# Kernel tuning notes

Measured on AMD Instinct MI355X. Metric: run time of the kernel, lower is better.

The kernel has to match this reference:

```python
import jax, jax.numpy as jnp
import numpy as np

N, E, D, H, C, G, L = 50000, 1250000, 128, 64, 10, 128, 2


def setup_inputs() -> dict:
    key = jax.random.key(0)
    ks = jax.random.split(key, 18)
    s = lambda fan_in: 1.0 / np.sqrt(fan_in)
    inp = {
        "x": jax.random.normal(ks[0], (N, D), dtype=jnp.float32),
        "edge_index": jax.random.randint(ks[1], (2, E), 0, N, dtype=jnp.int64),
        "batch": jnp.sort(jax.random.randint(ks[2], (N,), 0, G, dtype=jnp.int64)),
        # node embedding MLP (D->H->H)
        "emb_w1": jax.random.uniform(ks[3], (D, H), jnp.float32, -s(D), s(D)),
        "emb_b1": jnp.zeros((H,), jnp.float32),
        "emb_w2": jax.random.uniform(ks[4], (H, H), jnp.float32, -s(H), s(H)),
        "emb_b2": jnp.zeros((H,), jnp.float32),
        # per-conv-block params, stacked over L layers
        "rel_w": jax.random.uniform(ks[5], (L, H, H), jnp.float32, -s(H), s(H)),
        "rel_b": jnp.zeros((L, H), jnp.float32),
        "root_w": jax.random.uniform(ks[6], (L, H, H), jnp.float32, -s(H), s(H)),
        "post_w1": jax.random.uniform(ks[7], (L, H, H), jnp.float32, -s(H), s(H)),
        "post_b1": jnp.zeros((L, H), jnp.float32),
        "post_w2": jax.random.uniform(ks[8], (L, H, H), jnp.float32, -s(H), s(H)),
        "post_b2": jnp.zeros((L, H), jnp.float32),
        # classifier
        "cls_w": jax.random.uniform(ks[9], (H, C), jnp.float32, -s(H), s(H)),
        "cls_b": jnp.zeros((C,), jnp.float32),
    }
    return inp


def _mlp(h, w1, b1, w2, b2):
    # Linear -> relu -> (dropout: identity in eval) -> Linear
    return jax.nn.relu(h @ w1 + b1) @ w2 + b2


def reference(x, edge_index, batch, emb_w1, emb_b1, emb_w2, emb_b2,
              rel_w, rel_b, root_w, post_w1, post_b1, post_w2, post_b2,
              cls_w, cls_b):
    src, dst = edge_index[0], edge_index[1]
    h = _mlp(x, emb_w1, emb_b1, emb_w2, emb_b2)  # [N,H]
    deg = jax.ops.segment_sum(jnp.ones((E,), h.dtype), dst, num_segments=N)
    inv_deg = 1.0 / jnp.maximum(deg, 1.0)  # mean aggregation, isolated nodes -> 0
    for l in range(L):
        agg = jax.ops.segment_sum(h[src], dst, num_segments=N) * inv_deg[:, None]
        h = agg @ rel_w[l] + rel_b[l] + h @ root_w[l]  # GraphConv (lin_root bias-free)
        h = _mlp(h, post_w1[l], post_b1[l], post_w2[l], post_b2[l])
        h = jax.nn.relu(h)  # dropout is identity in eval
    cnt = jax.ops.segment_sum(jnp.ones((N,), h.dtype), batch, num_segments=G)
    pooled = jax.ops.segment_sum(h, batch, num_segments=G) / jnp.maximum(cnt, 1.0)[:, None]
    return pooled @ cls_w + cls_b  # [G,C]
```

## Files before the change

kernel.cpp:

```cpp
#include <hip/hip_runtime.h>

typedef unsigned int u32;
typedef unsigned short u16;

#define NN 50000
#define EE 1250000
#define DD 128
#define HH 64
#define NCLS 10
#define NG 128
#define MAXDEG 80

#define NTILES ((NN + 63) / 64)

#define PBUK 392
#define SBLK 128
#define CHUNK ((EE + SBLK - 1) / SBLK)
#define NDP  (PBUK * 128)

#define WT_LO  (8 * 4096)
#define WT_E1  (16 * 4096)
#define WT_E1L (WT_E1 + 8192)
#define WT_E2  (WT_E1 + 16384)
#define WT_E2L (WT_E2 + 4096)
#define WT_TOT (WT_E2 + 8192)


__device__ __forceinline__ u32 f2bf(float f) {
    u32 u = __float_as_uint(f);
    return (u + 0x7FFFu + ((u >> 16) & 1u)) >> 16;
}
__device__ __forceinline__ float bf2f(u16 v) {
    return __uint_as_float(((u32)v) << 16);
}

typedef __attribute__((ext_vector_type(8))) short bf16x8;
typedef __attribute__((ext_vector_type(4))) float f32x4;


__global__ __launch_bounds__(256) void k_wprep(
    const float* __restrict__ rel_w, const float* __restrict__ root_w,
    const float* __restrict__ pw1, const float* __restrict__ pw2,
    const float* __restrict__ ew1, const float* __restrict__ ew2,
    u16* __restrict__ wtb) {
    __shared__ float ldsf[128 * 65];
    const int t = threadIdx.x;
    const int m = blockIdx.x;
    if (m < 8) {
        const int layer = m >> 2, which = m & 3;
        const float* srcw =
            (which == 0 ? rel_w : which == 1 ? root_w : which == 2 ? pw1 : pw2)
            + (size_t)layer * HH * HH;
        #pragma unroll
        for (int r = 0; r < 16; ++r) {
            int idx = r * 256 + t;
            int k = idx >> 6, n = idx & 63;
            ldsf[k * 65 + n] = srcw[idx];
        }
        __syncthreads();
        #pragma unroll
        for (int r = 0; r < 16; ++r) {
            int idx = r * 256 + t;
            int n = idx >> 6, k = idx & 63;
            float v = ldsf[k * 65 + n];
            u16 hi = (u16)f2bf(v);
            u16 lo = (u16)f2bf(v - bf2f(hi));
            wtb[m * 4096 + idx] = hi;
            wtb[WT_LO + m * 4096 + idx] = lo;
        }
    } else if (m == 8) {
        #pragma unroll
        for (int r = 0; r < 32; ++r) {
            int idx = r * 256 + t;
            int k = idx >> 6, n = idx & 63;
            ldsf[k * 65 + n] = ew1[idx];
        }
        __syncthreads();
        #pragma unroll
        for (int r = 0; r < 32; ++r) {
            int idx = r * 256 + t;
            int n = idx >> 7, k = idx & 127;
            float v = ldsf[k * 65 + n];
            u16 hi = (u16)f2bf(v);
            u16 lo = (u16)f2bf(v - bf2f(hi));
            wtb[WT_E1 + idx] = hi;
            wtb[WT_E1L + idx] = lo;
        }
    } else {
        #pragma unroll
        for (int r = 0; r < 16; ++r) {
            int idx = r * 256 + t;
            int k = idx >> 6, n = idx & 63;
            ldsf[k * 65 + n] = ew2[idx];
        }
        __syncthreads();
        #pragma unroll
        for (int r = 0; r < 16; ++r) {
            int idx = r * 256 + t;
            int n = idx >> 6, k = idx & 63;
            float v = ldsf[k * 65 + n];
            u16 hi = (u16)f2bf(v);
            u16 lo = (u16)f2bf(v - bf2f(hi));
            wtb[WT_E2 + idx] = hi;
            wtb[WT_E2L + idx] = lo;
        }
    }
}


__global__ __launch_bounds__(256) void k_embed_psort(
    const float* __restrict__ x,
    const float* __restrict__ b1, const float* __restrict__ b2,
    const u16* __restrict__ wtb,
    u16* __restrict__ hb,
    const int* __restrict__ ei, u32* __restrict__ bedges,
    int* __restrict__ gboff, int* __restrict__ ghist) {
    __shared__ __align__(16) char smem[2 * 64 * 72 * 2];
    const int t = threadIdx.x;

    if (blockIdx.x < NTILES) {
        u16* acts0 = (u16*)smem;
        u16* acts1 = (u16*)smem + 64 * 72;
        const int l = t & 63;
        const int lr = l & 15, lg = l >> 4;
        const int rowb = (t >> 6) * 16;
        const int nb = blockIdx.x * 64;
        int nodeA = nb + rowb + lr;
        if (nodeA >= NN) nodeA = NN - 1;
        const float* xp = x + (size_t)nodeA * DD + lg * 8;

        f32x4 acc[4];
        #pragma unroll
        for (int tt = 0; tt < 4; ++tt) {
            float b = b1[tt * 16 + lr];
            acc[tt] = (f32x4){b, b, b, b};
        }
        #pragma unroll
        for (int kc = 0; kc < 4; ++kc) {
            float4 v0 = *(const float4*)(xp + kc * 32);
            float4 v1 = *(const float4*)(xp + kc * 32 + 4);
            float vv[8] = {v0.x, v0.y, v0.z, v0.w, v1.x, v1.y, v1.z, v1.w};
            bf16x8 xh, xl;
            #pragma unroll
            for (int j = 0; j < 8; ++j) {
                u16 hi = (u16)f2bf(vv[j]);
                xh[j] = (short)hi;
                xl[j] = (short)(u16)f2bf(vv[j] - bf2f(hi));
            }
            #pragma unroll
            for (int tt = 0; tt < 4; ++tt) {
                const u16* ph = wtb + WT_E1 + (tt * 16 + lr) * 128 + kc * 32 + lg * 8;
                const u16* pl = wtb + WT_E1L + (tt * 16 + lr) * 128 + kc * 32 + lg * 8;
                bf16x8 wh = *(const bf16x8*)ph;
                bf16x8 wl = *(const bf16x8*)pl;
                acc[tt] = __builtin_amdgcn_mfma_f32_16x16x32_bf16(xh, wh, acc[tt], 0, 0, 0);
                acc[tt] = __builtin_amdgcn_mfma_f32_16x16x32_bf16(xl, wh, acc[tt], 0, 0, 0);
                acc[tt] = __builtin_amdgcn_mfma_f32_16x16x32_bf16(xh, wl, acc[tt], 0, 0, 0);
            }
        }
        #pragma unroll
        for (int tt = 0; tt < 4; ++tt)
            #pragma unroll
            for (int r = 0; r < 4; ++r) {
                float v = fmaxf(acc[tt][r], 0.0f);
                u16 hi = (u16)f2bf(v);
                u16 lo = (u16)f2bf(v - bf2f(hi));
                acts0[(rowb + lg * 4 + r) * 72 + tt * 16 + lr] = hi;
                acts1[(rowb + lg * 4 + r) * 72 + tt * 16 + lr] = lo;
            }
        __syncthreads();

        bf16x8 c0h = *(const bf16x8*)&acts0[(rowb + lr) * 72 + lg * 8];
        bf16x8 c1h = *(const bf16x8*)&acts0[(rowb + lr) * 72 + 32 + lg * 8];
        bf16x8 c0l = *(const bf16x8*)&acts1[(rowb + lr) * 72 + lg * 8];
        bf16x8 c1l = *(const bf16x8*)&acts1[(rowb + lr) * 72 + 32 + lg * 8];
        f32x4 acc2[4];
        #pragma unroll
        for (int tt = 0; tt < 4; ++tt) {
            float b = b2[tt * 16 + lr];
            acc2[tt] = (f32x4){b, b, b, b};
        }
        #pragma unroll
        for (int tt = 0; tt < 4; ++tt) {
            const u16* ph = wtb + WT_E2 + (tt * 16 + lr) * 64 + lg * 8;
            const u16* pl = wtb + WT_E2L + (tt * 16 + lr) * 64 + lg * 8;
            bf16x8 wh0 = *(const bf16x8*)ph;
            bf16x8 wh1 = *(const bf16x8*)(ph + 32);
            bf16x8 wl0 = *(const bf16x8*)pl;
            bf16x8 wl1 = *(const bf16x8*)(pl + 32);
            acc2[tt] = __builtin_amdgcn_mfma_f32_16x16x32_bf16(c0h, wh0, acc2[tt], 0, 0, 0);
            acc2[tt] = __builtin_amdgcn_mfma_f32_16x16x32_bf16(c1h, wh1, acc2[tt], 0, 0, 0);
            acc2[tt] = __builtin_amdgcn_mfma_f32_16x16x32_bf16(c0l, wh0, acc2[tt], 0, 0, 0);
            acc2[tt] = __builtin_amdgcn_mfma_f32_16x16x32_bf16(c1l, wh1, acc2[tt], 0, 0, 0);
            acc2[tt] = __builtin_amdgcn_mfma_f32_16x16x32_bf16(c0h, wl0, acc2[tt], 0, 0, 0);
            acc2[tt] = __builtin_amdgcn_mfma_f32_16x16x32_bf16(c1h, wl1, acc2[tt], 0, 0, 0);
        }
        #pragma unroll
        for (int tt = 0; tt < 4; ++tt)
            #pragma unroll
            for (int r = 0; r < 4; ++r) {
                int node = nb + rowb + lg * 4 + r;
                if (node < NN)
                    hb[(size_t)node * HH + tt * 16 + lr] = (u16)f2bf(acc2[tt][r]);
            }
    } else {
        int* hist  = (int*)smem;
        int* boffS = hist + PBUK;
        int* wsum  = boffS + PBUK;
        const int cb = blockIdx.x - NTILES;
        const int base = cb * CHUNK;
        const int n = min(CHUNK, EE - base);

        for (int b = t; b < PBUK; b += 256) hist[b] = 0;
        __syncthreads();
        for (int i = t; i < n; i += 256) {
            int src = ei[base + i];
            int dst = ei[EE + base + i];
            if ((unsigned)src < NN && (unsigned)dst < NN)
                atomicAdd(&hist[dst >> 7], 1);
        }
        __syncthreads();
        int v = 0, h0 = 0;
        if (t < PBUK / 2) { h0 = hist[2 * t]; v = h0 + hist[2 * t + 1]; }
        int lane = t & 63, wd = t >> 6;
        int incl = v;
        #pragma unroll
        for (int d = 1; d < 64; d <<= 1) {
            int tt = __shfl_up(incl, d);
            if (lane >= d) incl += tt;
        }
        if (lane == 63) wsum[wd] = incl;
        __syncthreads();
        int woff = 0;
        for (int w = 0; w < wd; ++w) woff += wsum[w];
        if (t < PBUK / 2) {
            int excl = woff + incl - v;
            boffS[2 * t] = excl;
            boffS[2 * t + 1] = excl + h0;
        }
        __syncthreads();
        for (int b = t; b < PBUK; b += 256) {
            gboff[cb * PBUK + b] = boffS[b];
            ghist[cb * PBUK + b] = hist[b];
        }
        __syncthreads();
        for (int b = t; b < PBUK; b += 256) hist[b] = 0;
        __syncthreads();
        for (int i = t; i < n; i += 256) {
            int src = ei[base + i];
            int dst = ei[EE + base + i];
            if ((unsigned)src < NN && (unsigned)dst < NN) {
                int b = dst >> 7;
                int p = atomicAdd(&hist[b], 1);
                bedges[base + boffS[b] + p] = ((u32)src << 7) | (u32)(dst & 127);
            }
        }
    }
}


__global__ __launch_bounds__(256) void k_adj(const u32* __restrict__ bedges,
                                             const int* __restrict__ gboff,
                                             const int* __restrict__ ghist,
                                             u16* __restrict__ slots,
                                             int* __restrict__ deg,
                                             float* __restrict__ pooled,
                                             u16* __restrict__ hb) {
    __shared__ u16 ls[128 * MAXDEG];
    __shared__ int lc[128];
    const int b = blockIdx.x, t = threadIdx.x;
    const int lane = t & 63, wid = t >> 6;
    if (b < (NG * HH) / 256) pooled[b * 256 + t] = 0.0f;
    if (b == 0 && t < 32) ((u32*)hb)[NN * (HH / 2) + t] = 0;
    if (t < 128) lc[t] = 0;
    {
        const u32 sent = ((u32)NN << 16) | (u32)NN;
        u32* lsu = (u32*)ls;
        for (int i = t; i < 128 * MAXDEG / 2; i += 256) lsu[i] = sent;
    }
    __syncthreads();
    for (int sb = wid; sb < SBLK; sb += 4) {
        int off = gboff[sb * PBUK + b];
        int cnt = ghist[sb * PBUK + b];
        int gbase = sb * CHUNK + off;
        for (int i = lane; i < cnt; i += 64) {
            u32 p = bedges[gbase + i];
            int o = (int)(p & 127u);
            int src = (int)(p >> 7);
            int pos = atomicAdd(&lc[o], 1);
            if (pos < MAXDEG) ls[o * MAXDEG + pos] = (u16)src;
        }
    }
    __syncthreads();
    u32* gs = (u32*)(slots + (size_t)b * 128 * MAXDEG);
    const u32* lsu = (const u32*)ls;
    for (int i = t; i < 128 * MAXDEG / 2; i += 256) gs[i] = lsu[i];
    if (t < 128) deg[b * 128 + t] = lc[t];
}


__global__ __launch_bounds__(256) void k_agg(
    const u16* __restrict__ hb, const int* __restrict__ deg,
    const u16* __restrict__ slots, u16* __restrict__ aggb) {
    const int wid = threadIdx.x >> 6, lane = threadIdx.x & 63;
    const int half = lane >> 5, fl = lane & 31;
    const int n0 = blockIdx.x * 8 + wid * 2;
    if (n0 >= NN) return;
    const int n = n0 + half;
    const bool valid = n < NN;
    const int d = valid ? deg[n] : 0;
    const int m = min(d, MAXDEG);
    const int mp = (m + 15) & ~15;
    const u32* row = (const u32*)(slots + (size_t)n * MAXDEG);
    float s0 = 0.0f, s1 = 0.0f;
    for (int e = 0; e < mp; e += 16) {
        const u32* rp = row + (e >> 1);
        uint4 i0 = *(const uint4*)rp;
        uint4 i1 = *(const uint4*)(rp + 4);
        u32 v0 = *(const u32*)(hb + (size_t)(i0.x & 0xffffu) * HH + 2 * fl);
        u32 v1 = *(const u32*)(hb + (size_t)(i0.x >> 16)    * HH + 2 * fl);
        u32 v2 = *(const u32*)(hb + (size_t)(i0.y & 0xffffu) * HH + 2 * fl);
        u32 v3 = *(const u32*)(hb + (size_t)(i0.y >> 16)    * HH + 2 * fl);
        u32 v4 = *(const u32*)(hb + (size_t)(i0.z & 0xffffu) * HH + 2 * fl);
        u32 v5 = *(const u32*)(hb + (size_t)(i0.z >> 16)    * HH + 2 * fl);
        u32 v6 = *(const u32*)(hb + (size_t)(i0.w & 0xffffu) * HH + 2 * fl);
        u32 v7 = *(const u32*)(hb + (size_t)(i0.w >> 16)    * HH + 2 * fl);
        u32 v8 = *(const u32*)(hb + (size_t)(i1.x & 0xffffu) * HH + 2 * fl);
        u32 v9 = *(const u32*)(hb + (size_t)(i1.x >> 16)    * HH + 2 * fl);
        u32 va = *(const u32*)(hb + (size_t)(i1.y & 0xffffu) * HH + 2 * fl);
        u32 vb = *(const u32*)(hb + (size_t)(i1.y >> 16)    * HH + 2 * fl);
        u32 vc = *(const u32*)(hb + (size_t)(i1.z & 0xffffu) * HH + 2 * fl);
        u32 vd = *(const u32*)(hb + (size_t)(i1.z >> 16)    * HH + 2 * fl);
        u32 ve = *(const u32*)(hb + (size_t)(i1.w & 0xffffu) * HH + 2 * fl);
        u32 vf = *(const u32*)(hb + (size_t)(i1.w >> 16)    * HH + 2 * fl);
        s0 += ((bf2f((u16)(v0 & 0xffffu)) + bf2f((u16)(v1 & 0xffffu)))
             + (bf2f((u16)(v2 & 0xffffu)) + bf2f((u16)(v3 & 0xffffu))))
            + ((bf2f((u16)(v4 & 0xffffu)) + bf2f((u16)(v5 & 0xffffu)))
             + (bf2f((u16)(v6 & 0xffffu)) + bf2f((u16)(v7 & 0xffffu))));
        s0 += ((bf2f((u16)(v8 & 0xffffu)) + bf2f((u16)(v9 & 0xffffu)))
             + (bf2f((u16)(va & 0xffffu)) + bf2f((u16)(vb & 0xffffu))))
            + ((bf2f((u16)(vc & 0xffffu)) + bf2f((u16)(vd & 0xffffu)))
             + (bf2f((u16)(ve & 0xffffu)) + bf2f((u16)(vf & 0xffffu))));
        s1 += ((bf2f((u16)(v0 >> 16)) + bf2f((u16)(v1 >> 16)))
             + (bf2f((u16)(v2 >> 16)) + bf2f((u16)(v3 >> 16))))
            + ((bf2f((u16)(v4 >> 16)) + bf2f((u16)(v5 >> 16)))
             + (bf2f((u16)(v6 >> 16)) + bf2f((u16)(v7 >> 16))));
        s1 += ((bf2f((u16)(v8 >> 16)) + bf2f((u16)(v9 >> 16)))
             + (bf2f((u16)(va >> 16)) + bf2f((u16)(vb >> 16))))
            + ((bf2f((u16)(vc >> 16)) + bf2f((u16)(vd >> 16)))
             + (bf2f((u16)(ve >> 16)) + bf2f((u16)(vf >> 16))));
    }
    if (valid) {
        float inv = 1.0f / (float)max(d, 1);
        u32 p = f2bf(s0 * inv) | (f2bf(s1 * inv) << 16);
        ((u32*)aggb)[(size_t)n * (HH / 2) + fl] = p;
    }
}


__global__ __launch_bounds__(256) void k_dense(
    u16* __restrict__ hb, const u16* __restrict__ aggb,
    const u16* __restrict__ wt,
    const float* __restrict__ relb,
    const float* __restrict__ pb1, const float* __restrict__ pb2,
    const int* __restrict__ batch, float* __restrict__ pooled, int do_pool) {
    __shared__ __align__(16) u16 acts[2][64][72];
    const int t = threadIdx.x;
    const int w = t >> 6;
    const int l = t & 63;
    const int lr = l & 15, lg = l >> 4;
    const int rowb = w * 16;
    const int nb = blockIdx.x * 64;
    int nodeA = nb + rowb + lr;
    if (nodeA >= NN) nodeA = NN - 1;

    const u16* w_rel = wt;
    const u16* w_root = wt + 4096;
    const u16* w_p1  = wt + 2 * 4096;
    const u16* w_p2  = wt + 3 * 4096;

    const u16* agp = aggb + (size_t)nodeA * HH + lg * 8;
    const u16* hbp = hb   + (size_t)nodeA * HH + lg * 8;
    bf16x8 a0 = *(const bf16x8*)agp;
    bf16x8 a1 = *(const bf16x8*)(agp + 32);
    bf16x8 h0 = *(const bf16x8*)hbp;
    bf16x8 h1 = *(const bf16x8*)(hbp + 32);

    f32x4 acc[4];
    #pragma unroll
    for (int tt = 0; tt < 4; ++tt) {
        float b = relb[tt * 16 + lr];
        acc[tt] = (f32x4){b, b, b, b};
    }
    #pragma unroll
    for (int tt = 0; tt < 4; ++tt) {
        const u16* pr = w_rel  + (tt * 16 + lr) * 64 + lg * 8;
        const u16* po = w_root + (tt * 16 + lr) * 64 + lg * 8;
        acc[tt] = __builtin_amdgcn_mfma_f32_16x16x32_bf16(a0, *(const bf16x8*)pr,                acc[tt], 0, 0, 0);
        acc[tt] = __builtin_amdgcn_mfma_f32_16x16x32_bf16(a1, *(const bf16x8*)(pr + 32),         acc[tt], 0, 0, 0);
        acc[tt] = __builtin_amdgcn_mfma_f32_16x16x32_bf16(a0, *(const bf16x8*)(pr + WT_LO),      acc[tt], 0, 0, 0);
        acc[tt] = __builtin_amdgcn_mfma_f32_16x16x32_bf16(a1, *(const bf16x8*)(pr + WT_LO + 32), acc[tt], 0, 0, 0);
        acc[tt] = __builtin_amdgcn_mfma_f32_16x16x32_bf16(h0, *(const bf16x8*)po,                acc[tt], 0, 0, 0);
        acc[tt] = __builtin_amdgcn_mfma_f32_16x16x32_bf16(h1, *(const bf16x8*)(po + 32),         acc[tt], 0, 0, 0);
        acc[tt] = __builtin_amdgcn_mfma_f32_16x16x32_bf16(h0, *(const bf16x8*)(po + WT_LO),      acc[tt], 0, 0, 0);
        acc[tt] = __builtin_amdgcn_mfma_f32_16x16x32_bf16(h1, *(const bf16x8*)(po + WT_LO + 32), acc[tt], 0, 0, 0);
    }
    #pragma unroll
    for (int tt = 0; tt < 4; ++tt)
        #pragma unroll
        for (int r = 0; r < 4; ++r)
            acts[0][rowb + lg * 4 + r][tt * 16 + lr] = (u16)f2bf(acc[tt][r]);
    __syncthreads();

    bf16x8 c0 = *(const bf16x8*)&acts[0][rowb + lr][lg * 8];
    bf16x8 c1 = *(const bf16x8*)&acts[0][rowb + lr][32 + lg * 8];
    f32x4 acc2[4];
    #pragma unroll
    for (int tt = 0; tt < 4; ++tt) {
        float b = pb1[tt * 16 + lr];
        acc2[tt] = (f32x4){b, b, b, b};
    }
    #pragma unroll
    for (int tt = 0; tt < 4; ++tt) {
        const u16* pr = w_p1 + (tt * 16 + lr) * 64 + lg * 8;
        acc2[tt] = __builtin_amdgcn_mfma_f32_16x16x32_bf16(c0, *(const bf16x8*)pr,                acc2[tt], 0, 0, 0);
        acc2[tt] = __builtin_amdgcn_mfma_f32_16x16x32_bf16(c1, *(const bf16x8*)(pr + 32),         acc2[tt], 0, 0, 0);
        acc2[tt] = __builtin_amdgcn_mfma_f32_16x16x32_bf16(c0, *(const bf16x8*)(pr + WT_LO),      acc2[tt], 0, 0, 0);
        acc2[tt] = __builtin_amdgcn_mfma_f32_16x16x32_bf16(c1, *(const bf16x8*)(pr + WT_LO + 32), acc2[tt], 0, 0, 0);
    }
    #pragma unroll
    for (int tt = 0; tt < 4; ++tt)
        #pragma unroll
        for (int r = 0; r < 4; ++r)
            acts[1][rowb + lg * 4 + r][tt * 16 + lr] = (u16)f2bf(fmaxf(acc2[tt][r], 0.0f));
    __syncthreads();

    bf16x8 d0 = *(const bf16x8*)&acts[1][rowb + lr][lg * 8];
    bf16x8 d1 = *(const bf16x8*)&acts[1][rowb + lr][32 + lg * 8];
    f32x4 acc3[4];
    #pragma unroll
    for (int tt = 0; tt < 4; ++tt) {
        float b = pb2[tt * 16 + lr];
        acc3[tt] = (f32x4){b, b, b, b};
    }
    #pragma unroll
    for (int tt = 0; tt < 4; ++tt) {
        const u16* pr = w_p2 + (tt * 16 + lr) * 64 + lg * 8;
        acc3[tt] = __builtin_amdgcn_mfma_f32_16x16x32_bf16(d0, *(const bf16x8*)pr,                acc3[tt], 0, 0, 0);
        acc3[tt] = __builtin_amdgcn_mfma_f32_16x16x32_bf16(d1, *(const bf16x8*)(pr + 32),         acc3[tt], 0, 0, 0);
        acc3[tt] = __builtin_amdgcn_mfma_f32_16x16x32_bf16(d0, *(const bf16x8*)(pr + WT_LO),      acc3[tt], 0, 0, 0);
        acc3[tt] = __builtin_amdgcn_mfma_f32_16x16x32_bf16(d1, *(const bf16x8*)(pr + WT_LO + 32), acc3[tt], 0, 0, 0);
    }

    if (!do_pool) {
        #pragma unroll
        for (int tt = 0; tt < 4; ++tt)
            #pragma unroll
            for (int r = 0; r < 4; ++r) {
                int node = nb + rowb + lg * 4 + r;
                if (node < NN)
                    hb[(size_t)node * HH + tt * 16 + lr] = (u16)f2bf(fmaxf(acc3[tt][r], 0.0f));
            }
    } else {
        #pragma unroll
        for (int tt = 0; tt < 4; ++tt)
            #pragma unroll
            for (int r = 0; r < 4; ++r)
                acts[0][rowb + lg * 4 + r][tt * 16 + lr] = (u16)f2bf(fmaxf(acc3[tt][r], 0.0f));
        __syncthreads();
        if (t < HH) {
            const int f = t;
            const int n1 = min(64, NN - nb);
            int cur = batch[nb];
            float s = 0.0f;
            for (int i = 0; i < n1; ++i) {
                int g = batch[nb + i];
                if (g != cur) {
                    if ((unsigned)cur < NG) atomicAdd(&pooled[cur * HH + f], s);
                    s = 0.0f; cur = g;
                }
                s += bf2f(acts[0][i][f]);
            }
            if ((unsigned)cur < NG) atomicAdd(&pooled[cur * HH + f], s);
        }
    }
}


__global__ void k_cls(const float* __restrict__ pooled, const int* __restrict__ batch,
                      const float* __restrict__ w, const float* __restrict__ b,
                      float* __restrict__ out) {
    const int g = blockIdx.x;
    const int t = threadIdx.x;
    if (t >= NCLS) return;
    int lo = 0, hi = NN;
    while (lo < hi) { int mid = (lo + hi) >> 1; if (batch[mid] < g) lo = mid + 1; else hi = mid; }
    const int beg = lo;
    lo = 0; hi = NN;
    while (lo < hi) { int mid = (lo + hi) >> 1; if (batch[mid] < g + 1) lo = mid + 1; else hi = mid; }
    const int cnt = lo - beg;
    const float inv = 1.0f / (float)max(cnt, 1);
    float o = b[t];
    #pragma unroll 8
    for (int k = 0; k < HH; ++k) o += pooled[g * HH + k] * inv * w[k * NCLS + t];
    out[g * NCLS + t] = o;
}


extern "C" void kernel_launch(void* const* d_in, const int* in_sizes, int n_in,
                              void* d_out, int out_size, void* d_ws, size_t ws_size,
                              hipStream_t stream) {
    const float* x      = (const float*)d_in[0];
    const int*   ei     = (const int*)d_in[1];
    const int*   batch  = (const int*)d_in[2];
    const float* emb_w1 = (const float*)d_in[3];
    const float* emb_b1 = (const float*)d_in[4];
    const float* emb_w2 = (const float*)d_in[5];
    const float* emb_b2 = (const float*)d_in[6];
    const float* rel_w  = (const float*)d_in[7];
    const float* rel_b  = (const float*)d_in[8];
    const float* root_w = (const float*)d_in[9];
    const float* pw1    = (const float*)d_in[10];
    const float* pb1    = (const float*)d_in[11];
    const float* pw2    = (const float*)d_in[12];
    const float* pb2    = (const float*)d_in[13];
    const float* cls_w  = (const float*)d_in[14];
    const float* cls_b  = (const float*)d_in[15];
    float* out = (float*)d_out;

    char* ws = (char*)d_ws;
    size_t off = 0;
    auto alloc = [&](size_t bytes) -> void* {
        off = (off + 255) & ~(size_t)255;
        void* p = ws + off;
        off += bytes;
        return p;
    };
    u16*   hb     = (u16*)alloc((size_t)(NN + 1) * HH * 2);
    u16*   aggb   = (u16*)alloc((size_t)NN * HH * 2);
    u32*   bedges = (u32*)aggb;
    u16*   slots  = (u16*)alloc((size_t)NDP * MAXDEG * 2);
    int*   deg    = (int*)alloc((size_t)NDP * 4);
    int*   gboff  = (int*)alloc((size_t)SBLK * PBUK * 4);
    int*   ghist  = (int*)alloc((size_t)SBLK * PBUK * 4);
    float* pooled = (float*)alloc((size_t)NG * HH * 4);
    u16*   wtb    = (u16*)alloc((size_t)WT_TOT * 2);

    k_wprep<<<10, 256, 0, stream>>>(rel_w, root_w, pw1, pw2, emb_w1, emb_w2, wtb);
    k_embed_psort<<<NTILES + SBLK, 256, 0, stream>>>(
        x, emb_b1, emb_b2, wtb, hb, ei, bedges, gboff, ghist);
    k_adj<<<PBUK, 256, 0, stream>>>(bedges, gboff, ghist, slots, deg, pooled, hb);
    k_agg<<<(NN + 7) / 8, 256, 0, stream>>>(hb, deg, slots, aggb);
    k_dense<<<NTILES, 256, 0, stream>>>(hb, aggb, wtb, rel_b, pb1, pb2, batch, pooled, 0);
    k_agg<<<(NN + 7) / 8, 256, 0, stream>>>(hb, deg, slots, aggb);
    k_dense<<<NTILES, 256, 0, stream>>>(hb, aggb, wtb + 4 * 4096,
                                        rel_b + HH, pb1 + HH, pb2 + HH,
                                        batch, pooled, 1);
    k_cls<<<NG, 64, 0, stream>>>(pooled, batch, cls_w, cls_b, out);
}
```

Baseline: 285.9 us.

## Restructure neighbor aggregation to one wave per node with 16-byte gathers

The aggregation kernel now assigns one 64-lane wave per node. Each lane loads 8 bf16 features (16 bytes) of one of 8 neighbors at a time, and the partial sums are reduced across lanes with xor shuffles. This replaces the previous scheme, where half-waves did 4-byte gathers over 16 neighbors per iteration. The intent is wider, more efficient memory transactions and less padding waste for low-degree nodes, at the cost of a shuffle reduction and more blocks. Separately, the edge bucketing loops in the partition-sort kernel are unrolled by four so each thread has more edge-index loads in flight.

```diff
diff --git a/kernel.cpp b/kernel.cpp
--- a/kernel.cpp
+++ b/kernel.cpp
@@ -213,11 +213,17 @@
 
         for (int b = t; b < PBUK; b += 256) hist[b] = 0;
         __syncthreads();
-        for (int i = t; i < n; i += 256) {
-            int src = ei[base + i];
-            int dst = ei[EE + base + i];
-            if ((unsigned)src < NN && (unsigned)dst < NN)
-                atomicAdd(&hist[dst >> 7], 1);
+        for (int i0 = t; i0 < n; i0 += 1024) {
+            const int i1 = i0 + 256, i2 = i0 + 512, i3 = i0 + 768;
+            int sA = ei[base + i0], dA = ei[EE + base + i0];
+            int sB = -1, dB = 0, sC = -1, dC = 0, sD = -1, dD = 0;
+            if (i1 < n) { sB = ei[base + i1]; dB = ei[EE + base + i1]; }
+            if (i2 < n) { sC = ei[base + i2]; dC = ei[EE + base + i2]; }
+            if (i3 < n) { sD = ei[base + i3]; dD = ei[EE + base + i3]; }
+            if ((unsigned)sA < NN && (unsigned)dA < NN) atomicAdd(&hist[dA >> 7], 1);
+            if ((unsigned)sB < NN && (unsigned)dB < NN) atomicAdd(&hist[dB >> 7], 1);
+            if ((unsigned)sC < NN && (unsigned)dC < NN) atomicAdd(&hist[dC >> 7], 1);
+            if ((unsigned)sD < NN && (unsigned)dD < NN) atomicAdd(&hist[dD >> 7], 1);
         }
         __syncthreads();
         int v = 0, h0 = 0;
@@ -246,13 +252,32 @@
         __syncthreads();
         for (int b = t; b < PBUK; b += 256) hist[b] = 0;
         __syncthreads();
-        for (int i = t; i < n; i += 256) {
-            int src = ei[base + i];
-            int dst = ei[EE + base + i];
-            if ((unsigned)src < NN && (unsigned)dst < NN) {
-                int b = dst >> 7;
+        for (int i0 = t; i0 < n; i0 += 1024) {
+            const int i1 = i0 + 256, i2 = i0 + 512, i3 = i0 + 768;
+            int sA = ei[base + i0], dA = ei[EE + base + i0];
+            int sB = -1, dB = 0, sC = -1, dC = 0, sD = -1, dD = 0;
+            if (i1 < n) { sB = ei[base + i1]; dB = ei[EE + base + i1]; }
+            if (i2 < n) { sC = ei[base + i2]; dC = ei[EE + base + i2]; }
+            if (i3 < n) { sD = ei[base + i3]; dD = ei[EE + base + i3]; }
+            if ((unsigned)sA < NN && (unsigned)dA < NN) {
+                int b = dA >> 7;
                 int p = atomicAdd(&hist[b], 1);
-                bedges[base + boffS[b] + p] = ((u32)src << 7) | (u32)(dst & 127);
+                bedges[base + boffS[b] + p] = ((u32)sA << 7) | (u32)(dA & 127);
+            }
+            if ((unsigned)sB < NN && (unsigned)dB < NN) {
+                int b = dB >> 7;
+                int p = atomicAdd(&hist[b], 1);
+                bedges[base + boffS[b] + p] = ((u32)sB << 7) | (u32)(dB & 127);
+            }
+            if ((unsigned)sC < NN && (unsigned)dC < NN) {
+                int b = dC >> 7;
+                int p = atomicAdd(&hist[b], 1);
+                bedges[base + boffS[b] + p] = ((u32)sC << 7) | (u32)(dC & 127);
+            }
+            if ((unsigned)sD < NN && (unsigned)dD < NN) {
+                int b = dD >> 7;
+                int p = atomicAdd(&hist[b], 1);
+                bedges[base + boffS[b] + p] = ((u32)sD << 7) | (u32)(dD & 127);
             }
         }
     }
@@ -303,57 +328,35 @@
     const u16* __restrict__ hb, const int* __restrict__ deg,
     const u16* __restrict__ slots, u16* __restrict__ aggb) {
     const int wid = threadIdx.x >> 6, lane = threadIdx.x & 63;
-    const int half = lane >> 5, fl = lane & 31;
-    const int n0 = blockIdx.x * 8 + wid * 2;
-    if (n0 >= NN) return;
-    const int n = n0 + half;
-    const bool valid = n < NN;
-    const int d = valid ? deg[n] : 0;
+    const int n = blockIdx.x * 4 + wid;
+    if (n >= NN) return;
+    const int d = deg[n];
     const int m = min(d, MAXDEG);
-    const int mp = (m + 15) & ~15;
-    const u32* row = (const u32*)(slots + (size_t)n * MAXDEG);
-    float s0 = 0.0f, s1 = 0.0f;
-    for (int e = 0; e < mp; e += 16) {
-        const u32* rp = row + (e >> 1);
-        uint4 i0 = *(const uint4*)rp;
-        uint4 i1 = *(const uint4*)(rp + 4);
-        u32 v0 = *(const u32*)(hb + (size_t)(i0.x & 0xffffu) * HH + 2 * fl);
-        u32 v1 = *(const u32*)(hb + (size_t)(i0.x >> 16)    * HH + 2 * fl);
-        u32 v2 = *(const u32*)(hb + (size_t)(i0.y & 0xffffu) * HH + 2 * fl);
-        u32 v3 = *(const u32*)(hb + (size_t)(i0.y >> 16)    * HH + 2 * fl);
-        u32 v4 = *(const u32*)(hb + (size_t)(i0.z & 0xffffu) * HH + 2 * fl);
-        u32 v5 = *(const u32*)(hb + (size_t)(i0.z >> 16)    * HH + 2 * fl);
-        u32 v6 = *(const u32*)(hb + (size_t)(i0.w & 0xffffu) * HH + 2 * fl);
-        u32 v7 = *(const u32*)(hb + (size_t)(i0.w >> 16)    * HH + 2 * fl);
-        u32 v8 = *(const u32*)(hb + (size_t)(i1.x & 0xffffu) * HH + 2 * fl);
-        u32 v9 = *(const u32*)(hb + (size_t)(i1.x >> 16)    * HH + 2 * fl);
-        u32 va = *(const u32*)(hb + (size_t)(i1.y & 0xffffu) * HH + 2 * fl);
-        u32 vb = *(const u32*)(hb + (size_t)(i1.y >> 16)    * HH + 2 * fl);
-        u32 vc = *(const u32*)(hb + (size_t)(i1.z & 0xffffu) * HH + 2 * fl);
-        u32 vd = *(const u32*)(hb + (size_t)(i1.z >> 16)    * HH + 2 * fl);
-        u32 ve = *(const u32*)(hb + (size_t)(i1.w & 0xffffu) * HH + 2 * fl);
-        u32 vf = *(const u32*)(hb + (size_t)(i1.w >> 16)    * HH + 2 * fl);
-        s0 += ((bf2f((u16)(v0 & 0xffffu)) + bf2f((u16)(v1 & 0xffffu)))
-             + (bf2f((u16)(v2 & 0xffffu)) + bf2f((u16)(v3 & 0xffffu))))
-            + ((bf2f((u16)(v4 & 0xffffu)) + bf2f((u16)(v5 & 0xffffu)))
-             + (bf2f((u16)(v6 & 0xffffu)) + bf2f((u16)(v7 & 0xffffu))));
-        s0 += ((bf2f((u16)(v8 & 0xffffu)) + bf2f((u16)(v9 & 0xffffu)))
-             + (bf2f((u16)(va & 0xffffu)) + bf2f((u16)(vb & 0xffffu))))
-            + ((bf2f((u16)(vc & 0xffffu)) + bf2f((u16)(vd & 0xffffu)))
-             + (bf2f((u16)(ve & 0xffffu)) + bf2f((u16)(vf & 0xffffu))));
-        s1 += ((bf2f((u16)(v0 >> 16)) + bf2f((u16)(v1 >> 16)))
-             + (bf2f((u16)(v2 >> 16)) + bf2f((u16)(v3 >> 16))))
-            + ((bf2f((u16)(v4 >> 16)) + bf2f((u16)(v5 >> 16)))
-             + (bf2f((u16)(v6 >> 16)) + bf2f((u16)(v7 >> 16))));
-        s1 += ((bf2f((u16)(v8 >> 16)) + bf2f((u16)(v9 >> 16)))
-             + (bf2f((u16)(va >> 16)) + bf2f((u16)(vb >> 16))))
-            + ((bf2f((u16)(vc >> 16)) + bf2f((u16)(vd >> 16)))
-             + (bf2f((u16)(ve >> 16)) + bf2f((u16)(vf >> 16))));
-    }
-    if (valid) {
+    const int mp = (m + 7) & ~7;
+    const int eg = lane >> 3;
+    const int fo = (lane & 7) * 8;
+    const u16* row = slots + (size_t)n * MAXDEG;
+    float s[8] = {0, 0, 0, 0, 0, 0, 0, 0};
+    for (int e = 0; e < mp; e += 8) {
+        int src = row[e + eg];
+        uint4 v = *(const uint4*)(hb + (size_t)src * HH + fo);
+        s[0] += bf2f((u16)(v.x & 0xffffu)); s[1] += bf2f((u16)(v.x >> 16));
+        s[2] += bf2f((u16)(v.y & 0xffffu)); s[3] += bf2f((u16)(v.y >> 16));
+        s[4] += bf2f((u16)(v.z & 0xffffu)); s[5] += bf2f((u16)(v.z >> 16));
+        s[6] += bf2f((u16)(v.w & 0xffffu)); s[7] += bf2f((u16)(v.w >> 16));
+    }
+    #pragma unroll
+    for (int off = 8; off <= 32; off <<= 1)
+        #pragma unroll
+        for (int j = 0; j < 8; ++j)
+            s[j] += __shfl_xor(s[j], off, 64);
+    if (eg == 0) {
         float inv = 1.0f / (float)max(d, 1);
-        u32 p = f2bf(s0 * inv) | (f2bf(s1 * inv) << 16);
-        ((u32*)aggb)[(size_t)n * (HH / 2) + fl] = p;
+        u32 r0 = f2bf(s[0] * inv) | (f2bf(s[1] * inv) << 16);
+        u32 r1 = f2bf(s[2] * inv) | (f2bf(s[3] * inv) << 16);
+        u32 r2 = f2bf(s[4] * inv) | (f2bf(s[5] * inv) << 16);
+        u32 r3 = f2bf(s[6] * inv) | (f2bf(s[7] * inv) << 16);
+        *(uint4*)(aggb + (size_t)n * HH + fo) = make_uint4(r0, r1, r2, r3);
     }
 }
 
@@ -550,9 +553,9 @@
     k_embed_psort<<<NTILES + SBLK, 256, 0, stream>>>(
         x, emb_b1, emb_b2, wtb, hb, ei, bedges, gboff, ghist);
     k_adj<<<PBUK, 256, 0, stream>>>(bedges, gboff, ghist, slots, deg, pooled, hb);
-    k_agg<<<(NN + 7) / 8, 256, 0, stream>>>(hb, deg, slots, aggb);
+    k_agg<<<(NN + 3) / 4, 256, 0, stream>>>(hb, deg, slots, aggb);
     k_dense<<<NTILES, 256, 0, stream>>>(hb, aggb, wtb, rel_b, pb1, pb2, batch, pooled, 0);
-    k_agg<<<(NN + 7) / 8, 256, 0, stream>>>(hb, deg, slots, aggb);
+    k_agg<<<(NN + 3) / 4, 256, 0, stream>>>(hb, deg, slots, aggb);
     k_dense<<<NTILES, 256, 0, stream>>>(hb, aggb, wtb + 4 * 4096,
                                         rel_b + HH, pb1 + HH, pb2 + HH,
                                         batch, pooled, 1);
```

Result: slower. 299.5 us (+4.8%).
